# Kernel tuning notes

Measured on AMD Instinct MI355X. Metric: run time of the kernel, lower is better.

## Reference

```python
import jax, jax.numpy as jnp
import numpy as np

D, NH, NL, NP, DFF = 256, 8, 4, 4, 1024
HD = D // NH
SHAPES = np.array([[64, 64], [32, 32], [16, 16], [8, 8]], dtype=np.int32)  # (H, W) per level


def _layer_norm(x, g, b, eps=1e-5):
    mu = jnp.mean(x, -1, keepdims=True)
    var = jnp.mean((x - mu) ** 2, -1, keepdims=True)
    return (x - mu) * jax.lax.rsqrt(var + eps) * g + b


def _bilinear_sample(value_l, loc):
    # value_l: (N, H, W, NH, HD); loc: (N, Lq, NH, NP, 2) normalized to [0,1]
    # Matches F.grid_sample(align_corners=False, padding_mode='zeros') on grid 2*loc-1.
    N, H, W = value_l.shape[0], value_l.shape[1], value_l.shape[2]
    x = loc[..., 0] * W - 0.5
    y = loc[..., 1] * H - 0.5
    x0 = jnp.floor(x)
    y0 = jnp.floor(y)
    wx1 = x - x0
    wy1 = y - y0
    b_idx = jnp.arange(N)[:, None, None, None]
    h_idx = jnp.arange(NH)[None, None, :, None]

    def gather(yi, xi):
        valid = (yi >= 0) & (yi < H) & (xi >= 0) & (xi < W)
        yc = jnp.clip(yi, 0, H - 1).astype(jnp.int32)
        xc = jnp.clip(xi, 0, W - 1).astype(jnp.int32)
        v = value_l[b_idx, yc, xc, h_idx]  # (N, Lq, NH, NP, HD)
        return v * valid[..., None].astype(value_l.dtype)

    v00 = gather(y0, x0)
    v01 = gather(y0, x0 + 1)
    v10 = gather(y0 + 1, x0)
    v11 = gather(y0 + 1, x0 + 1)
    wx1 = wx1[..., None]
    wy1 = wy1[..., None]
    top = v00 * (1 - wx1) + v01 * wx1
    bot = v10 * (1 - wx1) + v11 * wx1
    return top * (1 - wy1) + bot * wy1  # (N, Lq, NH, NP, HD)


def setup_inputs() -> dict:
    key = jax.random.key(0)
    ks = jax.random.split(key, 24)
    N, Lq = 8, int(SHAPES.prod(axis=1).sum())  # 5440
    s = 0.02
    return {
        "src": jax.random.normal(ks[0], (N, Lq, D), jnp.float32),
        "pos": jax.random.normal(ks[1], (N, Lq, D), jnp.float32),
        "reference_points": jax.random.uniform(ks[2], (N, Lq, NL, 2), jnp.float32),
        "spatial_shapes": jnp.asarray(SHAPES),
        "W_value": s * jax.random.normal(ks[3], (D, D)),
        "b_value": jnp.zeros((D,)),
        "W_off": s * jax.random.normal(ks[4], (D, NH * NL * NP * 2)),
        "b_off": 0.5 * jax.random.normal(ks[5], (NH * NL * NP * 2,)),
        "W_attn": s * jax.random.normal(ks[6], (D, NH * NL * NP)),
        "b_attn": jnp.zeros((NH * NL * NP,)),
        "W_out": s * jax.random.normal(ks[7], (D, D)),
        "b_out": jnp.zeros((D,)),
        "ln1_g": jnp.ones((D,)),
        "ln1_b": jnp.zeros((D,)),
        "W1": s * jax.random.normal(ks[8], (D, DFF)),
        "b1": jnp.zeros((DFF,)),
        "W2": s * jax.random.normal(ks[9], (DFF, D)),
        "b2": jnp.zeros((D,)),
        "ln2_g": jnp.ones((D,)),
        "ln2_b": jnp.zeros((D,)),
    }


def reference(src, pos, reference_points, spatial_shapes,
              W_value, b_value, W_off, b_off, W_attn, b_attn, W_out, b_out,
              ln1_g, ln1_b, W1, b1, W2, b2, ln2_g, ln2_b):
    shapes = np.asarray(spatial_shapes)  # static (NL, 2)
    N, Lq = src.shape[0], src.shape[1]

    # --- MSDeformAttn ---
    query = src + pos
    value = (src @ W_value + b_value).reshape(N, Lq, NH, HD)
    offsets = (query @ W_off + b_off).reshape(N, Lq, NH, NL, NP, 2)
    attn = jax.nn.softmax((query @ W_attn + b_attn).reshape(N, Lq, NH, NL * NP), axis=-1)
    attn = attn.reshape(N, Lq, NH, NL, NP)
    # offset normalizer is (W, H) per level
    norm = jnp.asarray(np.stack([shapes[:, 1], shapes[:, 0]], -1), jnp.float32)  # (NL, 2)
    loc = reference_points[:, :, None, :, None, :] + offsets / norm[None, None, None, :, None, :]

    out = jnp.zeros((N, Lq, NH, HD), src.dtype)
    start = 0
    for l in range(NL):
        H, W = int(shapes[l, 0]), int(shapes[l, 1])
        v_l = jax.lax.dynamic_slice_in_dim(value, start, H * W, axis=1).reshape(N, H, W, NH, HD)
        sampled = _bilinear_sample(v_l, loc[:, :, :, l])  # (N, Lq, NH, NP, HD)
        out = out + jnp.einsum('nqhp,nqhpd->nqhd', attn[:, :, :, l], sampled)
        start += H * W
    src2 = out.reshape(N, Lq, D) @ W_out + b_out

    # --- residual + norm + FFN (dropout=0, eval) ---
    x = _layer_norm(src + src2, ln1_g, ln1_b)
    ffn = jax.nn.relu(x @ W1 + b1) @ W2 + b2
    return _layer_norm(x + ffn, ln2_g, ln2_b)
```

## Files before the change

### kernel.cpp

```cpp
#include <hip/hip_runtime.h>
#include <math.h>

#define LQ_ 5440
#define NB_ 8
#define NQ_ (NB_ * LQ_)
#define D_  256
#define NH_ 8
#define HD_ 32

typedef __attribute__((ext_vector_type(8))) short short8;
typedef __attribute__((ext_vector_type(4))) float f32x4;

__device__ __forceinline__ ushort f2bf(float f) {
    union { float f; unsigned u; } v; v.f = f;
    unsigned u = v.u;
    unsigned r = (u + 0x7FFFu + ((u >> 16) & 1u)) >> 16;
    return (ushort)r;
}

__device__ __forceinline__ void gload_lds16(const void* g, void* l) {
    __builtin_amdgcn_global_load_lds(
        (const __attribute__((address_space(1))) void*)g,
        (__attribute__((address_space(3))) void*)l, 16, 0, 0);
}

__device__ __forceinline__ void wg_barrier() {
    __builtin_amdgcn_sched_barrier(0);
    __builtin_amdgcn_s_barrier();
    __builtin_amdgcn_sched_barrier(0);
}

__global__ void make_bf_inputs(const float* __restrict__ src, const float* __restrict__ pos,
                               ushort* __restrict__ s_bf, ushort* __restrict__ q_bf) {
    const int i = blockIdx.x * blockDim.x + threadIdx.x;
    const float4 s = ((const float4*)src)[i];
    const float4 p = ((const float4*)pos)[i];
    ushort4 a, b;
    a.x = f2bf(s.x); a.y = f2bf(s.y); a.z = f2bf(s.z); a.w = f2bf(s.w);
    b.x = f2bf(s.x + p.x); b.y = f2bf(s.y + p.y); b.z = f2bf(s.z + p.z); b.w = f2bf(s.w + p.w);
    ((ushort4*)s_bf)[i] = a;
    ((ushort4*)q_bf)[i] = b;
}

__global__ void transpose_w(const float* __restrict__ W, ushort* __restrict__ Wt, int K, int N) {
    __shared__ float tile[32][33];
    const int bx = blockIdx.x;
    const int by = blockIdx.y;
    const int tx = threadIdx.x;
    const int ty = threadIdx.y;
    for (int i = ty; i < 32; i += 8)
        tile[i][tx] = W[(size_t)(by * 32 + i) * N + bx * 32 + tx];
    __syncthreads();
    for (int i = ty; i < 32; i += 8)
        Wt[(size_t)(bx * 32 + i) * K + by * 32 + tx] = f2bf(tile[tx][i]);
}

#define BM 128
#define BN 128
#define BK 64

__global__ __launch_bounds__(256)
void mfma_gemm(const ushort* __restrict__ A, const ushort* __restrict__ Bt,
               const float* __restrict__ bias, float* __restrict__ Cf,
               ushort* __restrict__ Cb, int N, int K, int relu) {
    __shared__ ushort lA[2][BM * BK];
    __shared__ ushort lB[2][BN * BK];
    const int t    = threadIdx.x;
    const int col0 = blockIdx.x * BN;
    const int row0 = blockIdx.y * BM;
    const int w    = t >> 6;
    const int lr   = t & 15;
    const int quad = (t >> 4) & 3;
    const int wm   = (w >> 1) * 64;
    const int wn   = (w & 1) * 64;

    f32x4 acc[4][4];
    #pragma unroll
    for (int i = 0; i < 4; ++i)
        #pragma unroll
        for (int j = 0; j < 4; ++j)
            acc[i][j] = (f32x4){0.f, 0.f, 0.f, 0.f};

    const int sr = t >> 3;
    const int sc = (t & 7) * 8;
    const size_t aoff = (size_t)(row0 + sr) * K + sc;
    const size_t boff = (size_t)(col0 + sr) * K + sc;
    const int wb = w * 1024;

    auto stage = [&](int buf, int k0) {
        char* la = (char*)lA[buf] + wb;
        char* lb = (char*)lB[buf] + wb;
        #pragma unroll
        for (int g = 0; g < 4; ++g) {
            gload_lds16(A  + aoff + k0 + (size_t)g * 32 * K, la + g * 4096);
            gload_lds16(Bt + boff + k0 + (size_t)g * 32 * K, lb + g * 4096);
        }
    };

    stage(0, 0);
    int cur = 0;
    for (int k0 = 0; k0 < K; k0 += BK) {
        if (k0 + BK < K) {
            stage(cur ^ 1, k0 + BK);
            asm volatile("s_waitcnt vmcnt(8)" ::: "memory");
        } else {
            asm volatile("s_waitcnt vmcnt(0)" ::: "memory");
        }
        wg_barrier();
        const ushort* pA = lA[cur];
        const ushort* pB = lB[cur];
        #pragma unroll
        for (int kk = 0; kk < 2; ++kk) {
            short8 af[4], bfr[4];
            #pragma unroll
            for (int i = 0; i < 4; ++i)
                af[i] = *(const short8*)(pA + (wm + i * 16 + lr) * BK + kk * 32 + quad * 8);
            #pragma unroll
            for (int j = 0; j < 4; ++j)
                bfr[j] = *(const short8*)(pB + (wn + j * 16 + lr) * BK + kk * 32 + quad * 8);
            #pragma unroll
            for (int i = 0; i < 4; ++i)
                #pragma unroll
                for (int j = 0; j < 4; ++j)
                    acc[i][j] = __builtin_amdgcn_mfma_f32_16x16x32_bf16(af[i], bfr[j], acc[i][j], 0, 0, 0);
        }
        wg_barrier();
        cur ^= 1;
    }

    #pragma unroll
    for (int j = 0; j < 4; ++j) {
        const int col = col0 + wn + j * 16 + lr;
        const float bb = bias ? bias[col] : 0.f;
        #pragma unroll
        for (int i = 0; i < 4; ++i) {
            const int rbase = row0 + wm + i * 16 + quad * 4;
            #pragma unroll
            for (int r = 0; r < 4; ++r) {
                float v = acc[i][j][r] + bb;
                if (relu) v = fmaxf(v, 0.f);
                if (Cf) Cf[(size_t)(rbase + r) * N + col] = v;
                else    Cb[(size_t)(rbase + r) * N + col] = f2bf(v);
            }
        }
    }
}

__global__ __launch_bounds__(256)
void msda_sample(const ushort* __restrict__ value, const float* __restrict__ comb,
                 const float* __restrict__ b_off, const float* __restrict__ b_attn,
                 const float* __restrict__ refp, ushort* __restrict__ out) {
    __shared__ int   s_addr[256][4];
    __shared__ float s_w[256][4];

    const int t   = threadIdx.x;
    const int tq  = t >> 7;
    const int u   = t & 127;
    const int bid = blockIdx.x;
    const int swz = (bid & 7) * (NQ_ / 2 / 8) + (bid >> 3);
    const int nq  = swz * 2 + tq;
    const int n   = nq / LQ_;

    {
        const int h = u >> 4;
        const int p = u & 15;
        const int l = p >> 2;

        const int starts[4] = {0, 4096, 5120, 5376};
        const int Wl = 64 >> l;

        float a = comb[(size_t)nq * 384 + 256 + u] + b_attn[u];
        float m = a;
        #pragma unroll
        for (int o = 8; o > 0; o >>= 1) m = fmaxf(m, __shfl_xor(m, o));
        float e = __expf(a - m);
        float s = e;
        #pragma unroll
        for (int o = 8; o > 0; o >>= 1) s += __shfl_xor(s, o);
        const float wgt = e / s;

        const float rx = refp[(size_t)nq * 8 + l * 2 + 0];
        const float ry = refp[(size_t)nq * 8 + l * 2 + 1];
        const float ox = comb[(size_t)nq * 384 + u * 2 + 0] + b_off[u * 2 + 0];
        const float oy = comb[(size_t)nq * 384 + u * 2 + 1] + b_off[u * 2 + 1];

        const float fw = (float)Wl;
        const float x  = (rx + ox / fw) * fw - 0.5f;
        const float y  = (ry + oy / fw) * fw - 0.5f;
        const float x0f = floorf(x), y0f = floorf(y);
        const int   x0 = (int)x0f, y0 = (int)y0f;
        const float wx1 = x - x0f, wy1 = y - y0f;
        const float wx0 = 1.f - wx1, wy0 = 1.f - wy1;

        const float xm0 = (x0 >= 0 && x0 < Wl) ? 1.f : 0.f;
        const float xm1 = (x0 + 1 >= 0 && x0 + 1 < Wl) ? 1.f : 0.f;
        const float ym0 = (y0 >= 0 && y0 < Wl) ? 1.f : 0.f;
        const float ym1 = (y0 + 1 >= 0 && y0 + 1 < Wl) ? 1.f : 0.f;

        const int x0c = min(max(x0, 0), Wl - 1);
        const int x1c = min(max(x0 + 1, 0), Wl - 1);
        const int y0c = min(max(y0, 0), Wl - 1);
        const int y1c = min(max(y0 + 1, 0), Wl - 1);

        const int base = (n * LQ_ + starts[l]) * 512 + h * 64;
        s_addr[t][0] = base + (y0c * Wl + x0c) * 512;
        s_addr[t][1] = base + (y0c * Wl + x1c) * 512;
        s_addr[t][2] = base + (y1c * Wl + x0c) * 512;
        s_addr[t][3] = base + (y1c * Wl + x1c) * 512;
        s_w[t][0] = wgt * wy0 * wx0 * ym0 * xm0;
        s_w[t][1] = wgt * wy0 * wx1 * ym0 * xm1;
        s_w[t][2] = wgt * wy1 * wx0 * ym1 * xm0;
        s_w[t][3] = wgt * wy1 * wx1 * ym1 * xm1;
    }
    __syncthreads();

    {
        const int h   = u >> 4;
        const int d2  = u & 15;
        const int sb  = tq * 128 + h * 16;
        const uint dby = (uint)(d2 * 4);
        const char* vbase = (const char*)value;

        float acc0 = 0.f, acc1 = 0.f;
        #pragma unroll 8
        for (int p = 0; p < 16; ++p) {
            const int*   ap = s_addr[sb + p];
            const float* wp = s_w[sb + p];
            #pragma unroll
            for (int c = 0; c < 4; ++c) {
                const uint v = *(const uint*)(vbase + ((uint)ap[c] + dby));
                const float w = wp[c];
                union { uint u; float f; } lo, hi;
                lo.u = v << 16;
                hi.u = v & 0xffff0000u;
                acc0 = fmaf(lo.f, w, acc0);
                acc1 = fmaf(hi.f, w, acc1);
            }
        }
        const uint packed = (uint)f2bf(acc0) | ((uint)f2bf(acc1) << 16);
        ((uint*)out)[(size_t)nq * 128 + u] = packed;
    }
}

__global__ __launch_bounds__(256)
void add_ln(const float* __restrict__ a, const float* __restrict__ b,
            const float* __restrict__ g, const float* __restrict__ be,
            float* __restrict__ xf, ushort* __restrict__ xb) {
    const int row  = blockIdx.x * 4 + (threadIdx.x >> 6);
    const int lane = threadIdx.x & 63;
    const size_t base = (size_t)row * 256 + lane * 4;

    const float4 av = *(const float4*)(a + base);
    const float4 bv = *(const float4*)(b + base);
    float4 x;
    x.x = av.x + bv.x; x.y = av.y + bv.y; x.z = av.z + bv.z; x.w = av.w + bv.w;

    float s = x.x + x.y + x.z + x.w;
    #pragma unroll
    for (int o = 32; o > 0; o >>= 1) s += __shfl_xor(s, o);
    const float mu = s * (1.f / 256.f);

    float4 dx;
    dx.x = x.x - mu; dx.y = x.y - mu; dx.z = x.z - mu; dx.w = x.w - mu;
    float vv = dx.x * dx.x + dx.y * dx.y + dx.z * dx.z + dx.w * dx.w;
    #pragma unroll
    for (int o = 32; o > 0; o >>= 1) vv += __shfl_xor(vv, o);
    const float rstd = rsqrtf(vv * (1.f / 256.f) + 1e-5f);

    const float4 gv  = *(const float4*)(g  + lane * 4);
    const float4 bev = *(const float4*)(be + lane * 4);
    float4 y;
    y.x = dx.x * rstd * gv.x + bev.x;
    y.y = dx.y * rstd * gv.y + bev.y;
    y.z = dx.z * rstd * gv.z + bev.z;
    y.w = dx.w * rstd * gv.w + bev.w;

    *(float4*)(xf + base) = y;
    if (xb) {
        ushort4 yb;
        yb.x = f2bf(y.x); yb.y = f2bf(y.y); yb.z = f2bf(y.z); yb.w = f2bf(y.w);
        *(ushort4*)(xb + base) = yb;
    }
}

extern "C" void kernel_launch(void* const* d_in, const int* in_sizes, int n_in,
                              void* d_out, int out_size, void* d_ws, size_t ws_size,
                              hipStream_t stream) {
    const float* src     = (const float*)d_in[0];
    const float* pos     = (const float*)d_in[1];
    const float* refp    = (const float*)d_in[2];
    const float* W_value = (const float*)d_in[4];
    const float* b_value = (const float*)d_in[5];
    const float* W_off   = (const float*)d_in[6];
    const float* b_off   = (const float*)d_in[7];
    const float* W_attn  = (const float*)d_in[8];
    const float* b_attn  = (const float*)d_in[9];
    const float* W_out   = (const float*)d_in[10];
    const float* b_out   = (const float*)d_in[11];
    const float* ln1g    = (const float*)d_in[12];
    const float* ln1b    = (const float*)d_in[13];
    const float* W1      = (const float*)d_in[14];
    const float* b1      = (const float*)d_in[15];
    const float* W2      = (const float*)d_in[16];
    const float* b2      = (const float*)d_in[17];
    const float* ln2g    = (const float*)d_in[18];
    const float* ln2b    = (const float*)d_in[19];
    float* out = (float*)d_out;
    char*  ws  = (char*)d_ws;

    const size_t SZ_BF = (size_t)NQ_ * 256 * 2;
    const size_t SZ_F  = (size_t)NQ_ * 256 * 4;
    ushort* s_bf    = (ushort*)(ws);
    ushort* q_bf    = (ushort*)(ws + SZ_BF);
    ushort* val_bf  = (ushort*)(ws + 2 * SZ_BF);
    float*  comb    = (float*) (ws + 3 * SZ_BF);
    ushort* samp_bf = (ushort*)(ws + 4 * SZ_BF + SZ_F);
    ushort* h_bf    = (ushort*)(ws);
    ushort* x_bf    = (ushort*)(ws + 3 * SZ_BF + SZ_F);
    char*   wbase   = ws + 5 * SZ_BF + SZ_F;
    ushort* Wv_t    = (ushort*)(wbase);
    ushort* Woff_t  = (ushort*)(wbase + 131072);
    ushort* Wattn_t = (ushort*)(wbase + 262144);
    ushort* Wout_t  = (ushort*)(wbase + 327680);
    ushort* W1_t    = (ushort*)(wbase + 458752);
    ushort* W2_t    = (ushort*)(wbase + 983040);
    char*   fbase   = wbase + 1507328;
    float*  src2    = (float*)(fbase);
    float*  xf      = (float*)(fbase + SZ_F);

    make_bf_inputs<<<dim3((NQ_ * 256 / 4) / 256), 256, 0, stream>>>(src, pos, s_bf, q_bf);
    transpose_w<<<dim3(8, 8),  dim3(32, 8), 0, stream>>>(W_value, Wv_t,   256, 256);
    transpose_w<<<dim3(8, 8),  dim3(32, 8), 0, stream>>>(W_off,   Woff_t, 256, 256);
    transpose_w<<<dim3(4, 8),  dim3(32, 8), 0, stream>>>(W_attn,  Wattn_t,256, 128);
    transpose_w<<<dim3(8, 8),  dim3(32, 8), 0, stream>>>(W_out,   Wout_t, 256, 256);
    transpose_w<<<dim3(32, 8), dim3(32, 8), 0, stream>>>(W1,      W1_t,   256, 1024);
    transpose_w<<<dim3(8, 32), dim3(32, 8), 0, stream>>>(W2,      W2_t,   1024, 256);

    const int MT = NQ_ / BM;

    mfma_gemm<<<dim3(2, MT), 256, 0, stream>>>(s_bf, Wv_t, b_value, nullptr, val_bf, 256, 256, 0);
    mfma_gemm<<<dim3(3, MT), 256, 0, stream>>>(q_bf, Woff_t, nullptr, comb, nullptr, 384, 256, 0);
    msda_sample<<<dim3(NQ_ / 2), 256, 0, stream>>>(val_bf, comb, b_off, b_attn, refp, samp_bf);
    mfma_gemm<<<dim3(2, MT), 256, 0, stream>>>(samp_bf, Wout_t, b_out, src2, nullptr, 256, 256, 0);
    add_ln<<<dim3(NQ_ / 4), 256, 0, stream>>>(src, src2, ln1g, ln1b, xf, x_bf);
    mfma_gemm<<<dim3(8, MT), 256, 0, stream>>>(x_bf, W1_t, b1, nullptr, h_bf, 1024, 256, 1);
    mfma_gemm<<<dim3(2, MT), 256, 0, stream>>>(h_bf, W2_t, b2, src2, nullptr, 256, 1024, 0);
    add_ln<<<dim3(NQ_ / 4), 256, 0, stream>>>(xf, src2, ln2g, ln2b, out, nullptr);
}
```

Measured before the change: 498.9 us.

## Merge prep kernels, remap GEMM workgroups across XCDs, swizzle MSDA LDS tables

Folds the bf16 input conversion and all six weight transposes into one prep launch, cutting six kernel launches. Remaps GEMM workgroup indices so consecutive tiles land on the same XCD (blocks dispatched round-robin over 8 chiplets), aiming for better L2 reuse of A/B tiles. Swizzles the sampling kernel's LDS address/weight table rows by XOR of head and point index to reduce bank conflicts. These are three unrelated tweaks bundled together.

After: 487.8 us. 2.2% less time.

```diff
diff --git a/kernel.cpp b/kernel.cpp
--- a/kernel.cpp
+++ b/kernel.cpp
@@ -30,24 +30,44 @@
     __builtin_amdgcn_sched_barrier(0);
 }
 
-__global__ void make_bf_inputs(const float* __restrict__ src, const float* __restrict__ pos,
-                               ushort* __restrict__ s_bf, ushort* __restrict__ q_bf) {
-    const int i = blockIdx.x * blockDim.x + threadIdx.x;
-    const float4 s = ((const float4*)src)[i];
-    const float4 p = ((const float4*)pos)[i];
-    ushort4 a, b;
-    a.x = f2bf(s.x); a.y = f2bf(s.y); a.z = f2bf(s.z); a.w = f2bf(s.w);
-    b.x = f2bf(s.x + p.x); b.y = f2bf(s.y + p.y); b.z = f2bf(s.z + p.z); b.w = f2bf(s.w + p.w);
-    ((ushort4*)s_bf)[i] = a;
-    ((ushort4*)q_bf)[i] = b;
-}
-
-__global__ void transpose_w(const float* __restrict__ W, ushort* __restrict__ Wt, int K, int N) {
+#define TPREP_ 736
+
+__global__ __launch_bounds__(256)
+void prep(const float* __restrict__ src, const float* __restrict__ pos,
+          ushort* __restrict__ s_bf, ushort* __restrict__ q_bf,
+          const float* __restrict__ Wv, const float* __restrict__ Woff,
+          const float* __restrict__ Wattn, const float* __restrict__ Wout,
+          const float* __restrict__ W1, const float* __restrict__ W2,
+          ushort* __restrict__ Wv_t, ushort* __restrict__ Woff_t,
+          ushort* __restrict__ Wattn_t, ushort* __restrict__ Wout_t,
+          ushort* __restrict__ W1_t, ushort* __restrict__ W2_t) {
     __shared__ float tile[32][33];
-    const int bx = blockIdx.x;
-    const int by = blockIdx.y;
-    const int tx = threadIdx.x;
-    const int ty = threadIdx.y;
+    const int bid = blockIdx.x;
+    const int tid = threadIdx.x;
+
+    if (bid >= TPREP_) {
+        const int i = (bid - TPREP_) * 256 + tid;
+        const float4 s = ((const float4*)src)[i];
+        const float4 p = ((const float4*)pos)[i];
+        ushort4 a, b;
+        a.x = f2bf(s.x); a.y = f2bf(s.y); a.z = f2bf(s.z); a.w = f2bf(s.w);
+        b.x = f2bf(s.x + p.x); b.y = f2bf(s.y + p.y);
+        b.z = f2bf(s.z + p.z); b.w = f2bf(s.w + p.w);
+        ((ushort4*)s_bf)[i] = a;
+        ((ushort4*)q_bf)[i] = b;
+        return;
+    }
+
+    const float* W; ushort* Wt; int K, N, bx, by;
+    if (bid < 64)       { W = Wv;    Wt = Wv_t;    K = 256;  N = 256;  bx = bid % 8;         by = bid / 8; }
+    else if (bid < 128) { W = Woff;  Wt = Woff_t;  K = 256;  N = 256;  bx = (bid-64) % 8;    by = (bid-64) / 8; }
+    else if (bid < 160) { W = Wattn; Wt = Wattn_t; K = 256;  N = 128;  bx = (bid-128) % 4;   by = (bid-128) / 4; }
+    else if (bid < 224) { W = Wout;  Wt = Wout_t;  K = 256;  N = 256;  bx = (bid-160) % 8;   by = (bid-160) / 8; }
+    else if (bid < 480) { W = W1;    Wt = W1_t;    K = 256;  N = 1024; bx = (bid-224) % 32;  by = (bid-224) / 32; }
+    else                { W = W2;    Wt = W2_t;    K = 1024; N = 256;  bx = (bid-480) % 8;   by = (bid-480) / 8; }
+
+    const int tx = tid & 31;
+    const int ty = tid >> 5;
     for (int i = ty; i < 32; i += 8)
         tile[i][tx] = W[(size_t)(by * 32 + i) * N + bx * 32 + tx];
     __syncthreads();
@@ -65,9 +85,19 @@
                ushort* __restrict__ Cb, int N, int K, int relu) {
     __shared__ ushort lA[2][BM * BK];
     __shared__ ushort lB[2][BN * BK];
-    const int t    = threadIdx.x;
-    const int col0 = blockIdx.x * BN;
-    const int row0 = blockIdx.y * BM;
+    const int t = threadIdx.x;
+
+    const int nt   = gridDim.x;
+    const int nwg  = nt * gridDim.y;
+    const int flat = blockIdx.y * nt + blockIdx.x;
+    const int xc   = flat & 7;
+    const int sl   = flat >> 3;
+    const int q8   = nwg >> 3;
+    const int rm8  = nwg & 7;
+    const int wi   = (xc < rm8 ? xc * (q8 + 1) : rm8 * (q8 + 1) + (xc - rm8) * q8) + sl;
+    const int col0 = (wi % nt) * BN;
+    const int row0 = (wi / nt) * BM;
+
     const int w    = t >> 6;
     const int lr   = t & 15;
     const int quad = (t >> 4) & 3;
@@ -150,8 +180,9 @@
 void msda_sample(const ushort* __restrict__ value, const float* __restrict__ comb,
                  const float* __restrict__ b_off, const float* __restrict__ b_attn,
                  const float* __restrict__ refp, ushort* __restrict__ out) {
-    __shared__ int   s_addr[256][4];
-    __shared__ float s_w[256][4];
+    __shared__ int s_blob[2048];
+    int*   s_addr = s_blob;
+    float* s_w    = (float*)(s_blob + 1024);
 
     const int t   = threadIdx.x;
     const int tq  = t >> 7;
@@ -203,29 +234,31 @@
         const int y1c = min(max(y0 + 1, 0), Wl - 1);
 
         const int base = (n * LQ_ + starts[l]) * 512 + h * 64;
-        s_addr[t][0] = base + (y0c * Wl + x0c) * 512;
-        s_addr[t][1] = base + (y0c * Wl + x1c) * 512;
-        s_addr[t][2] = base + (y1c * Wl + x0c) * 512;
-        s_addr[t][3] = base + (y1c * Wl + x1c) * 512;
-        s_w[t][0] = wgt * wy0 * wx0 * ym0 * xm0;
-        s_w[t][1] = wgt * wy0 * wx1 * ym0 * xm1;
-        s_w[t][2] = wgt * wy1 * wx0 * ym1 * xm0;
-        s_w[t][3] = wgt * wy1 * wx1 * ym1 * xm1;
+        const int idx  = (tq << 7) + (p << 3) + (h ^ (p & 7));
+        s_addr[idx * 4 + 0] = base + (y0c * Wl + x0c) * 512;
+        s_addr[idx * 4 + 1] = base + (y0c * Wl + x1c) * 512;
+        s_addr[idx * 4 + 2] = base + (y1c * Wl + x0c) * 512;
+        s_addr[idx * 4 + 3] = base + (y1c * Wl + x1c) * 512;
+        s_w[idx * 4 + 0] = wgt * wy0 * wx0 * ym0 * xm0;
+        s_w[idx * 4 + 1] = wgt * wy0 * wx1 * ym0 * xm1;
+        s_w[idx * 4 + 2] = wgt * wy1 * wx0 * ym1 * xm0;
+        s_w[idx * 4 + 3] = wgt * wy1 * wx1 * ym1 * xm1;
     }
     __syncthreads();
 
     {
         const int h   = u >> 4;
         const int d2  = u & 15;
-        const int sb  = tq * 128 + h * 16;
+        const int tqb = tq << 7;
         const uint dby = (uint)(d2 * 4);
         const char* vbase = (const char*)value;
 
         float acc0 = 0.f, acc1 = 0.f;
         #pragma unroll 8
         for (int p = 0; p < 16; ++p) {
-            const int*   ap = s_addr[sb + p];
-            const float* wp = s_w[sb + p];
+            const int row = tqb + (p << 3) + (h ^ (p & 7));
+            const int*   ap = s_addr + row * 4;
+            const float* wp = s_w    + row * 4;
             #pragma unroll
             for (int c = 0; c < 4; ++c) {
                 const uint v = *(const uint*)(vbase + ((uint)ap[c] + dby));
@@ -328,13 +361,9 @@
     float*  src2    = (float*)(fbase);
     float*  xf      = (float*)(fbase + SZ_F);
 
-    make_bf_inputs<<<dim3((NQ_ * 256 / 4) / 256), 256, 0, stream>>>(src, pos, s_bf, q_bf);
-    transpose_w<<<dim3(8, 8),  dim3(32, 8), 0, stream>>>(W_value, Wv_t,   256, 256);
-    transpose_w<<<dim3(8, 8),  dim3(32, 8), 0, stream>>>(W_off,   Woff_t, 256, 256);
-    transpose_w<<<dim3(4, 8),  dim3(32, 8), 0, stream>>>(W_attn,  Wattn_t,256, 128);
-    transpose_w<<<dim3(8, 8),  dim3(32, 8), 0, stream>>>(W_out,   Wout_t, 256, 256);
-    transpose_w<<<dim3(32, 8), dim3(32, 8), 0, stream>>>(W1,      W1_t,   256, 1024);
-    transpose_w<<<dim3(8, 32), dim3(32, 8), 0, stream>>>(W2,      W2_t,   1024, 256);
+    prep<<<dim3(TPREP_ + (NQ_ * 256 / 4) / 256), 256, 0, stream>>>(
+        src, pos, s_bf, q_bf, W_value, W_off, W_attn, W_out, W1, W2,
+        Wv_t, Woff_t, Wattn_t, Wout_t, W1_t, W2_t);
 
     const int MT = NQ_ / BM;
 
```
